# Kernel optimization log

Hardware: AMD Instinct MI355X
Metric: run time of the kernel (lower is better)

## Reference

```python
import jax, jax.numpy as jnp
import numpy as np

N, T, D_IN = 100000, 64, 2
H = 64            # hidden_channels
HEADS = 2
D_OUT = 2
E = 1000000
NEG_SLOPE = 0.2


def setup_inputs() -> dict:
    key = jax.random.key(0)
    ks = jax.random.split(key, 12)
    s = 0.05
    return {
        "x": jax.random.normal(ks[0], (N, T, D_IN), dtype=jnp.float32),
        "edge_index": jax.random.randint(ks[1], (2, E), 0, N, dtype=jnp.int64),
        # LSTM params (PyTorch gate order i,f,g,o)
        "w_ih": jax.random.normal(ks[2], (4 * H, D_IN), dtype=jnp.float32) * s,
        "w_hh": jax.random.normal(ks[3], (4 * H, H), dtype=jnp.float32) * s,
        "b_ih": jax.random.normal(ks[4], (4 * H,), dtype=jnp.float32) * s,
        "b_hh": jax.random.normal(ks[5], (4 * H,), dtype=jnp.float32) * s,
        # GATConv params (heads=2, concat=False)
        "gat_w": jax.random.normal(ks[6], (HEADS * H, H), dtype=jnp.float32) * s,
        "att_src": jax.random.normal(ks[7], (HEADS, H), dtype=jnp.float32) * s,
        "att_dst": jax.random.normal(ks[8], (HEADS, H), dtype=jnp.float32) * s,
        "gat_b": jax.random.normal(ks[9], (H,), dtype=jnp.float32) * s,
        # output head
        "lin_w": jax.random.normal(ks[10], (D_OUT, H), dtype=jnp.float32) * s,
        "lin_b": jax.random.normal(ks[11], (D_OUT,), dtype=jnp.float32) * s,
    }


def _lstm_last_h(x, w_ih, w_hh, b_ih, b_hh):
    """Single-layer batch_first LSTM; returns final hidden state [N, H]."""
    n = x.shape[0]
    # Precompute input projections for all timesteps: [T, N, 4H]
    x_proj = jnp.einsum('ntd,gd->tng', x, w_ih) + (b_ih + b_hh)

    def step(carry, xt):
        h, c = carry
        gates = xt + h @ w_hh.T                       # [N, 4H]
        i, f, g, o = jnp.split(gates, 4, axis=-1)
        i = jax.nn.sigmoid(i)
        f = jax.nn.sigmoid(f)
        g = jnp.tanh(g)
        o = jax.nn.sigmoid(o)
        c = f * c + i * g
        h = o * jnp.tanh(c)
        return (h, c), None

    h0 = jnp.zeros((n, H), dtype=x.dtype)
    (h_n, _), _ = jax.lax.scan(step, (h0, h0), x_proj)
    return h_n


def _gat_conv(x, edge_index, gat_w, att_src, att_dst, gat_b):
    """PyG GATConv, heads=2, concat=False (mean over heads), add_self_loops=True."""
    n = x.shape[0]
    # add self-loops
    loops = jnp.arange(n, dtype=edge_index.dtype)
    src = jnp.concatenate([edge_index[0], loops])
    dst = jnp.concatenate([edge_index[1], loops])

    xh = (x @ gat_w.T).reshape(n, HEADS, H)           # [N, heads, H]
    a_src = jnp.einsum('nhd,hd->nh', xh, att_src)     # [N, heads]
    a_dst = jnp.einsum('nhd,hd->nh', xh, att_dst)

    e = a_src[src] + a_dst[dst]                       # [Etot, heads]
    e = jax.nn.leaky_relu(e, NEG_SLOPE)
    # segment softmax over incoming edges of each destination node
    m = jax.ops.segment_max(e, dst, num_segments=n)
    e = jnp.exp(e - m[dst])
    z = jax.ops.segment_sum(e, dst, num_segments=n)
    alpha = e / z[dst]                                # [Etot, heads]

    msg = xh[src] * alpha[:, :, None]                 # [Etot, heads, H]
    out = jax.ops.segment_sum(msg, dst, num_segments=n)  # [N, heads, H]
    return out.mean(axis=1) + gat_b                   # concat=False -> mean


def reference(x, edge_index, w_ih, w_hh, b_ih, b_hh, gat_w, att_src, att_dst, gat_b, lin_w, lin_b):
    t_out = _lstm_last_h(x, w_ih, w_hh, b_ih, b_hh)           # [N, H]
    s_out = jax.nn.relu(_gat_conv(t_out, edge_index, gat_w, att_src, att_dst, gat_b))
    return jax.nn.sigmoid(s_out @ lin_w.T + lin_b)            # [N, D_OUT]
```

## Files before the change

kernel.cpp:

```cpp
#include <hip/hip_runtime.h>
#include <hip/hip_bf16.h>
#include <string.h>

#define NN 100000
#define TT 64
#define EE 1000000
#define LOG2E 1.44269504088896340736f

typedef __attribute__((ext_vector_type(8))) short bf16x8;
typedef __attribute__((ext_vector_type(4))) float f32x4;
typedef unsigned int u32;
typedef unsigned short u16;

__device__ __forceinline__ float bflo(u32 u) { return __builtin_bit_cast(float, u << 16); }
__device__ __forceinline__ float bfhi(u32 u) { return __builtin_bit_cast(float, u & 0xffff0000u); }
__device__ __forceinline__ u16 f2bf(float f) {
    u32 u = __builtin_bit_cast(u32, f);
    return (u16)((u + 0x7fffu + ((u >> 16) & 1u)) >> 16);
}
__device__ __forceinline__ u32 pack2(float a, float b) {
    return (u32)f2bf(a) | ((u32)f2bf(b) << 16);
}
__device__ __forceinline__ u32 pack2c(float a, float b) {
    __hip_bfloat162 t = __float22bfloat162_rn(make_float2(a, b));
    u32 r;
    __builtin_memcpy(&r, &t, 4);
    return r;
}
__device__ __forceinline__ float ex2(float x) { return __builtin_amdgcn_exp2f(x); }
__device__ __forceinline__ float fast_rcp(float x) { return __builtin_amdgcn_rcpf(x); }
#define MFMA16(A, B, C) __builtin_amdgcn_mfma_f32_16x16x32_bf16((A), (B), (C), 0, 0, 0)

__global__ __launch_bounds__(256)
__attribute__((amdgpu_waves_per_eu(2, 8))) void lstm_kernel(
    const float* __restrict__ x,
    const float* __restrict__ w_ih,
    const float* __restrict__ w_hh,
    const float* __restrict__ b_ih,
    const float* __restrict__ b_hh,
    u16* __restrict__ h_out)
{
    __shared__ __align__(16) u16 h_sh[2][64 * 72];
    __shared__ __align__(8) u32 x_lds[64 * 10];

    const int tid = threadIdx.x;
    const int wv = tid >> 6, lane = tid & 63;
    const int q = lane >> 4, cl = lane & 15;

    bf16x8 aI0, aI1, aF0, aF1, aG0, aG1, aO0, aO1;
    bf16x8 wxI, wxF, wxG, wxO;
    {
        const int rbase = wv * 16 + cl;
#define LOAD_A(D0, D1, G, SC)                                                \
        {                                                                    \
            const float* wr_ = w_hh + ((G) * 64 + rbase) * 64 + q * 8;       \
            float4 u0 = *(const float4*)(wr_);                               \
            float4 u1 = *(const float4*)(wr_ + 4);                           \
            uint4 t;                                                         \
            t.x = pack2(u0.x * (SC), u0.y * (SC));                           \
            t.y = pack2(u0.z * (SC), u0.w * (SC));                           \
            t.z = pack2(u1.x * (SC), u1.y * (SC));                           \
            t.w = pack2(u1.z * (SC), u1.w * (SC));                           \
            D0 = __builtin_bit_cast(bf16x8, t);                              \
            float4 v0 = *(const float4*)(wr_ + 32);                          \
            float4 v1 = *(const float4*)(wr_ + 36);                          \
            t.x = pack2(v0.x * (SC), v0.y * (SC));                           \
            t.y = pack2(v0.z * (SC), v0.w * (SC));                           \
            t.z = pack2(v1.x * (SC), v1.y * (SC));                           \
            t.w = pack2(v1.z * (SC), v1.w * (SC));                           \
            D1 = __builtin_bit_cast(bf16x8, t);                              \
        }
        LOAD_A(aI0, aI1, 0, LOG2E)
        LOAD_A(aF0, aF1, 1, LOG2E)
        LOAD_A(aG0, aG1, 2, 2.f * LOG2E)
        LOAD_A(aO0, aO1, 3, LOG2E)
#undef LOAD_A
#define LOAD_WT(D, G, SC)                                                    \
        {                                                                    \
            uint4 t = make_uint4(0u, 0u, 0u, 0u);                            \
            if (q == 0) {                                                    \
                int row = (G) * 64 + rbase;                                  \
                t.x = pack2(w_ih[row * 2 + 0] * (SC), w_ih[row * 2 + 1] * (SC)); \
                t.y = (u32)f2bf((b_ih[row] + b_hh[row]) * (SC));             \
            }                                                                \
            D = __builtin_bit_cast(bf16x8, t);                               \
        }
        LOAD_WT(wxI, 0, LOG2E)
        LOAD_WT(wxF, 1, LOG2E)
        LOAD_WT(wxG, 2, 2.f * LOG2E)
        LOAD_WT(wxO, 3, LOG2E)
#undef LOAD_WT
    }

    {
        u32* z = (u32*)h_sh[0];
        for (int i = tid; i < 2304; i += 256) z[i] = 0u;
    }

    const int nodeL = tid >> 2, f4 = tid & 3;
    int gnd = blockIdx.x * 64 + nodeL;
    gnd = gnd < NN ? gnd : NN - 1;
    const float* px = x + ((size_t)gnd * 64 + f4 * 2) * 2;
    float4 xr = *(const float4*)px;

    float cst[16];
#pragma unroll
    for (int i = 0; i < 16; ++i) cst[i] = 0.f;

    const f32x4 zero4 = {0.f, 0.f, 0.f, 0.f};
    const int rd16 = cl * 72 + q * 8;
    const int wr16 = cl * 72 + wv * 16 + q * 4;
    const int x16 = cl * 10;

    auto step = [&](const u16* hr_, u16* hw_, int SL) {
#pragma unroll
        for (int ct = 0; ct < 4; ++ct) {
            bf16x8 bh0 = *(const bf16x8*)(hr_ + ct * 1152 + rd16);
            bf16x8 bh1 = *(const bf16x8*)(hr_ + ct * 1152 + rd16 + 32);
            uint4 xt;
            xt.x = x_lds[ct * 160 + x16 + SL];
            xt.y = 0x00003F80u;
            xt.z = 0u; xt.w = 0u;
            bf16x8 bx = __builtin_bit_cast(bf16x8, xt);
            f32x4 accI, accF, accG, accO;
            accI = MFMA16(aI0, bh0, zero4);
            accI = MFMA16(aI1, bh1, accI);
            accI = MFMA16(wxI, bx, accI);
            accF = MFMA16(aF0, bh0, zero4);
            accF = MFMA16(aF1, bh1, accF);
            accF = MFMA16(wxF, bx, accF);
            accG = MFMA16(aG0, bh0, zero4);
            accG = MFMA16(aG1, bh1, accG);
            accG = MFMA16(wxG, bx, accG);
            accO = MFMA16(aO0, bh0, zero4);
            accO = MFMA16(aO1, bh1, accO);
            accO = MFMA16(wxO, bx, accO);
            float h0, h1, h2, h3;
#define ACT(R, HOUT)                                                       \
            {                                                              \
                float a_ = ex2(-accI[R]);                                  \
                float b_ = ex2(-accG[R]);                                  \
                float d_ = ex2(-accF[R]);                                  \
                float e_ = ex2(-accO[R]);                                  \
                float P = (1.f + a_) * (1.f + b_);                         \
                float D1 = 1.f + d_;                                       \
                float num = fmaf(cst[ct * 4 + R], P, (1.f - b_) * D1);     \
                float cc = num * fast_rcp(P * D1);                         \
                cst[ct * 4 + R] = cc;                                      \
                float t_ = ex2(-2.f * LOG2E * cc);                         \
                float R2 = (1.f + e_) * (1.f + t_);                        \
                HOUT = (1.f - t_) * fast_rcp(R2);                          \
            }
            ACT(0, h0) ACT(1, h1) ACT(2, h2) ACT(3, h3)
#undef ACT
            *((uint2*)(hw_ + ct * 1152 + wr16)) =
                make_uint2(pack2c(h0, h1), pack2c(h2, h3));
        }
    };

    for (int c = 0; c < 8; ++c) {
        *((uint2*)(x_lds + nodeL * 10 + f4 * 2)) =
            make_uint2(pack2c(xr.x, xr.y), pack2c(xr.z, xr.w));
        if (c < 7) xr = *(const float4*)(px + (c + 1) * 16);
        __syncthreads();
        for (int s2 = 0; s2 < 4; ++s2) {
            step(h_sh[0], h_sh[1], s2 * 2);
            __syncthreads();
            step(h_sh[1], h_sh[0], s2 * 2 + 1);
            __syncthreads();
        }
    }
#pragma unroll
    for (int i = 0; i < 8; ++i) {
        int id = i * 256 + tid;
        int row = id >> 5, col2 = (id & 31) * 2;
        int nd = blockIdx.x * 64 + row;
        if (nd < NN) {
            u32 u = *(const u32*)(h_sh[0] + row * 72 + col2);
            *((u32*)(h_out + (size_t)nd * 64 + col2)) = u;
        }
    }
}

__global__ void watt_kernel(const float* __restrict__ gat_w,
                            const float* __restrict__ att_src,
                            const float* __restrict__ att_dst,
                            float* __restrict__ watt) {
    int tid = threadIdx.x;
    int v = tid >> 6, k = tid & 63;
    int head = v & 1;
    const float* att = (v < 2) ? att_src : att_dst;
    float acc = 0.f;
#pragma unroll 8
    for (int d = 0; d < 64; ++d)
        acc = fmaf(att[head * 64 + d], gat_w[(head * 64 + d) * 64 + k], acc);
    watt[v * 64 + k] = acc;
}

__global__ __launch_bounds__(256, 2) void xh_kernel(
    const u16* __restrict__ h,
    const float* __restrict__ gat_w,
    const float* __restrict__ watt,
    u32* __restrict__ xh,
    float2* __restrict__ asrc,
    float2* __restrict__ adst)
{
    __shared__ __align__(16) u16 afrag[16 * 64 * 8];
    const int tid = threadIdx.x;
    const int wv = tid >> 6, lane = tid & 63;
    const int q = lane >> 4, cl = lane & 15;

    for (int f = wv; f < 16; f += 4) {
        int t = f >> 1, kh = f & 1;
        const float4* s4 = (const float4*)(gat_w + (t * 16 + cl) * 64 + kh * 32 + q * 8);
        float4 u0 = s4[0], u1 = s4[1];
        u16* d = afrag + (f * 64 + lane) * 8;
        d[0] = f2bf(u0.x); d[1] = f2bf(u0.y); d[2] = f2bf(u0.z); d[3] = f2bf(u0.w);
        d[4] = f2bf(u1.x); d[5] = f2bf(u1.y); d[6] = f2bf(u1.z); d[7] = f2bf(u1.w);
    }
    uint4 wa0u = make_uint4(0u, 0u, 0u, 0u), wa1u = wa0u;
    if (cl < 4) {
        const float* wp = watt + cl * 64;
        float4 a = *(const float4*)(wp + q * 8), b = *(const float4*)(wp + q * 8 + 4);
        wa0u = make_uint4(pack2(a.x, a.y), pack2(a.z, a.w), pack2(b.x, b.y), pack2(b.z, b.w));
        a = *(const float4*)(wp + 32 + q * 8); b = *(const float4*)(wp + 32 + q * 8 + 4);
        wa1u = make_uint4(pack2(a.x, a.y), pack2(a.z, a.w), pack2(b.x, b.y), pack2(b.z, b.w));
    }
    int node = blockIdx.x * 64 + wv * 16 + cl;
    node = node < NN ? node : NN - 1;
    const u16* hp = h + (size_t)node * 64;
    bf16x8 bh0 = *(const bf16x8*)(hp + q * 8);
    bf16x8 bh1 = *(const bf16x8*)(hp + 32 + q * 8);
    __syncthreads();

    const f32x4 zero4 = {0.f, 0.f, 0.f, 0.f};
    f32x4 acc[8];
#pragma unroll
    for (int t = 0; t < 8; ++t) {
        bf16x8 a0 = *(const bf16x8*)(afrag + ((t * 2 + 0) * 64 + lane) * 8);
        bf16x8 a1 = *(const bf16x8*)(afrag + ((t * 2 + 1) * 64 + lane) * 8);
        acc[t] = MFMA16(a0, bh0, zero4);
        acc[t] = MFMA16(a1, bh1, acc[t]);
    }
    f32x4 aw = MFMA16(__builtin_bit_cast(bf16x8, wa0u), bh0, zero4);
    aw = MFMA16(__builtin_bit_cast(bf16x8, wa1u), bh1, aw);

#pragma unroll
    for (int t = 0; t < 4; ++t) {
        uint4 o;
        o.x = pack2c(acc[t][0], acc[t + 4][0]);
        o.y = pack2c(acc[t][1], acc[t + 4][1]);
        o.z = pack2c(acc[t][2], acc[t + 4][2]);
        o.w = pack2c(acc[t][3], acc[t + 4][3]);
        *((uint4*)(xh + (size_t)node * 64 + t * 16 + q * 4)) = o;
    }
    if (q == 0) {
        asrc[node] = make_float2(aw[0], aw[1]);
        adst[node] = make_float2(aw[2], aw[3]);
    }
}

__global__ void hist_kernel(const int* __restrict__ ei, u32* __restrict__ deg) {
    int e = blockIdx.x * 256 + threadIdx.x;
    if (e < EE) atomicAdd(&deg[ei[EE + e]], 1u);
}

__global__ void scan1_kernel(u32* rp, u32* bsum) {
    __shared__ u32 tmp[256];
    int i = blockIdx.x * 256 + threadIdx.x;
    u32 v = (i < NN) ? rp[i] : 0u;
    tmp[threadIdx.x] = v;
    __syncthreads();
    for (int off = 1; off < 256; off <<= 1) {
        u32 t = (threadIdx.x >= (u32)off) ? tmp[threadIdx.x - off] : 0u;
        __syncthreads();
        tmp[threadIdx.x] += t;
        __syncthreads();
    }
    if (i < NN) rp[i] = tmp[threadIdx.x] - v;
    if (threadIdx.x == 255) bsum[blockIdx.x] = tmp[255];
}

__global__ void scan2_kernel(u32* bsum) {
    __shared__ u32 tmp[512];
    int tid = threadIdx.x;
    u32 v = (tid < 391) ? bsum[tid] : 0u;
    tmp[tid] = v;
    __syncthreads();
    for (int off = 1; off < 512; off <<= 1) {
        u32 t = (tid >= off) ? tmp[tid - off] : 0u;
        __syncthreads();
        tmp[tid] += t;
        __syncthreads();
    }
    if (tid < 391) bsum[tid] = tmp[tid] - v;
}

__global__ void scan3_kernel(u32* rp, const u32* __restrict__ bsum, u32* __restrict__ cursor) {
    int i = blockIdx.x * 256 + threadIdx.x;
    if (i < NN) {
        u32 v = rp[i] + bsum[blockIdx.x];
        rp[i] = v;
        cursor[i] = v;
    }
    if (blockIdx.x == 0 && threadIdx.x == 0) rp[NN] = EE;
}

__global__ void fill_kernel(const int* __restrict__ ei, u32* __restrict__ cursor,
                            int* __restrict__ csr) {
    int e = blockIdx.x * 256 + threadIdx.x;
    if (e < EE) {
        int s = ei[e], d = ei[EE + e];
        u32 p = atomicAdd(&cursor[d], 1u);
        csr[p] = s;
    }
}

__global__ __launch_bounds__(256) void gather_kernel(
    const u32* __restrict__ xh,
    const float2* __restrict__ asrc,
    const float2* __restrict__ adst,
    const u32* __restrict__ rp,
    const int* __restrict__ csr,
    const float* __restrict__ gat_b,
    const float* __restrict__ lin_w,
    const float* __restrict__ lin_b,
    float2* __restrict__ out)
{
    int wv = threadIdx.x >> 6, lane = threadIdx.x & 63;
    int node = blockIdx.x * 4 + wv;
    float2 ad = adst[node];
    float2 as = asrc[node];
    float e0 = as.x + ad.x; e0 = e0 > 0.f ? e0 : 0.2f * e0;
    float e1 = as.y + ad.y; e1 = e1 > 0.f ? e1 : 0.2f * e1;
    float w0 = ex2(LOG2E * e0);
    float w1 = ex2(LOG2E * e1);
    u32 u = xh[(size_t)node * 64 + lane];
    float acc0 = w0 * bflo(u), acc1 = w1 * bfhi(u);
    float z0 = w0, z1 = w1;
    u32 beg = rp[node], end = rp[node + 1];
    u32 p = beg;
    for (; p + 2 <= end; p += 2) {
        int s0 = csr[p], s1 = csr[p + 1];
        float2 A0 = asrc[s0], A1 = asrc[s1];
        u32 u0 = xh[(size_t)s0 * 64 + lane];
        u32 u1 = xh[(size_t)s1 * 64 + lane];
        float f00 = A0.x + ad.x; f00 = f00 > 0.f ? f00 : 0.2f * f00;
        float f01 = A0.y + ad.y; f01 = f01 > 0.f ? f01 : 0.2f * f01;
        float f10 = A1.x + ad.x; f10 = f10 > 0.f ? f10 : 0.2f * f10;
        float f11 = A1.y + ad.y; f11 = f11 > 0.f ? f11 : 0.2f * f11;
        float v00 = ex2(LOG2E * f00);
        float v01 = ex2(LOG2E * f01);
        float v10 = ex2(LOG2E * f10);
        float v11 = ex2(LOG2E * f11);
        acc0 = fmaf(v00, bflo(u0), acc0);
        acc1 = fmaf(v01, bfhi(u0), acc1);
        acc0 = fmaf(v10, bflo(u1), acc0);
        acc1 = fmaf(v11, bfhi(u1), acc1);
        z0 += v00 + v10;
        z1 += v01 + v11;
    }
    if (p < end) {
        int s = csr[p];
        float2 a2 = asrc[s];
        u32 uu = xh[(size_t)s * 64 + lane];
        float f0 = a2.x + ad.x; f0 = f0 > 0.f ? f0 : 0.2f * f0;
        float f1 = a2.y + ad.y; f1 = f1 > 0.f ? f1 : 0.2f * f1;
        float v0 = ex2(LOG2E * f0);
        float v1 = ex2(LOG2E * f1);
        acc0 = fmaf(v0, bflo(uu), acc0);
        acc1 = fmaf(v1, bfhi(uu), acc1);
        z0 += v0;
        z1 += v1;
    }
    float od = 0.5f * (acc0 * fast_rcp(z0) + acc1 * fast_rcp(z1)) + gat_b[lane];
    od = fmaxf(od, 0.f);
    float p0 = od * lin_w[lane];
    float p1 = od * lin_w[64 + lane];
#pragma unroll
    for (int off = 32; off > 0; off >>= 1) {
        p0 += __shfl_xor(p0, off);
        p1 += __shfl_xor(p1, off);
    }
    if (lane == 0) {
        float y0 = fast_rcp(1.f + ex2(-LOG2E * (p0 + lin_b[0])));
        float y1 = fast_rcp(1.f + ex2(-LOG2E * (p1 + lin_b[1])));
        out[node] = make_float2(y0, y1);
    }
}

extern "C" void kernel_launch(void* const* d_in, const int* in_sizes, int n_in,
                              void* d_out, int out_size, void* d_ws, size_t ws_size,
                              hipStream_t stream) {
    const float* x = (const float*)d_in[0];
    const int* ei = (const int*)d_in[1];
    const float* w_ih = (const float*)d_in[2];
    const float* w_hh = (const float*)d_in[3];
    const float* b_ih = (const float*)d_in[4];
    const float* b_hh = (const float*)d_in[5];
    const float* gat_w = (const float*)d_in[6];
    const float* att_src = (const float*)d_in[7];
    const float* att_dst = (const float*)d_in[8];
    const float* gat_b = (const float*)d_in[9];
    const float* lin_w = (const float*)d_in[10];
    const float* lin_b = (const float*)d_in[11];

    char* w = (char*)d_ws;
    u16* h = (u16*)(w);
    u32* xh = (u32*)(w + 12800000);
    float2* asrc = (float2*)(w + 38400000);
    float2* adst = (float2*)(w + 39200000);
    u32* rp = (u32*)(w + 40000000);
    u32* cursor = (u32*)(w + 40400128);
    u32* bsum = (u32*)(w + 40800128);
    int* csr = (int*)(w + 40802176);
    float* watt = (float*)(w + 44802176);

    (void)hipMemsetAsync(rp, 0, (NN + 1) * sizeof(u32), stream);
    lstm_kernel<<<1563, 256, 0, stream>>>(x, w_ih, w_hh, b_ih, b_hh, h);
    watt_kernel<<<1, 256, 0, stream>>>(gat_w, att_src, att_dst, watt);
    xh_kernel<<<1563, 256, 0, stream>>>(h, gat_w, watt, xh, asrc, adst);
    hist_kernel<<<(EE + 255) / 256, 256, 0, stream>>>(ei, rp);
    scan1_kernel<<<391, 256, 0, stream>>>(rp, bsum);
    scan2_kernel<<<1, 512, 0, stream>>>(bsum);
    scan3_kernel<<<391, 256, 0, stream>>>(rp, bsum, cursor);
    fill_kernel<<<(EE + 255) / 256, 256, 0, stream>>>(ei, cursor, csr);
    gather_kernel<<<NN / 4, 256, 0, stream>>>(xh, asrc, adst, rp, csr, gat_b, lin_w, lin_b,
                                              (float2*)d_out);
}
```

Measured before the change: 783.8 us.

## Process two independent 64-node groups per LSTM block to interleave recurrences

```diff
diff --git a/kernel.cpp b/kernel.cpp
--- a/kernel.cpp
+++ b/kernel.cpp
@@ -40,8 +40,8 @@
     const float* __restrict__ b_hh,
     u16* __restrict__ h_out)
 {
-    __shared__ __align__(16) u16 h_sh[2][64 * 72];
-    __shared__ __align__(8) u32 x_lds[64 * 10];
+    __shared__ __align__(16) u16 h_sh[2][2][64 * 72];
+    __shared__ __align__(8) u32 x_lds[2][64 * 10];
 
     const int tid = threadIdx.x;
     const int wv = tid >> 6, lane = tid & 63;
@@ -93,32 +93,37 @@
     }
 
     {
-        u32* z = (u32*)h_sh[0];
-        for (int i = tid; i < 2304; i += 256) z[i] = 0u;
+        u32* z0 = (u32*)h_sh[0][0];
+        u32* z1 = (u32*)h_sh[1][0];
+        for (int i = tid; i < 2304; i += 256) { z0[i] = 0u; z1[i] = 0u; }
     }
 
     const int nodeL = tid >> 2, f4 = tid & 3;
-    int gnd = blockIdx.x * 64 + nodeL;
-    gnd = gnd < NN ? gnd : NN - 1;
-    const float* px = x + ((size_t)gnd * 64 + f4 * 2) * 2;
-    float4 xr = *(const float4*)px;
-
-    float cst[16];
-#pragma unroll
-    for (int i = 0; i < 16; ++i) cst[i] = 0.f;
+    int gndA = blockIdx.x * 128 + nodeL;
+    int gndB = gndA + 64;
+    gndA = gndA < NN ? gndA : NN - 1;
+    gndB = gndB < NN ? gndB : NN - 1;
+    const float* pxA = x + ((size_t)gndA * 64 + f4 * 2) * 2;
+    const float* pxB = x + ((size_t)gndB * 64 + f4 * 2) * 2;
+    float4 xrA = *(const float4*)pxA;
+    float4 xrB = *(const float4*)pxB;
+
+    float cstA[16], cstB[16];
+#pragma unroll
+    for (int i = 0; i < 16; ++i) { cstA[i] = 0.f; cstB[i] = 0.f; }
 
     const f32x4 zero4 = {0.f, 0.f, 0.f, 0.f};
     const int rd16 = cl * 72 + q * 8;
     const int wr16 = cl * 72 + wv * 16 + q * 4;
     const int x16 = cl * 10;
 
-    auto step = [&](const u16* hr_, u16* hw_, int SL) {
+    auto step = [&](const u16* hr_, u16* hw_, int SL, float* cst_, const u32* xl_) {
 #pragma unroll
         for (int ct = 0; ct < 4; ++ct) {
             bf16x8 bh0 = *(const bf16x8*)(hr_ + ct * 1152 + rd16);
             bf16x8 bh1 = *(const bf16x8*)(hr_ + ct * 1152 + rd16 + 32);
             uint4 xt;
-            xt.x = x_lds[ct * 160 + x16 + SL];
+            xt.x = xl_[ct * 160 + x16 + SL];
             xt.y = 0x00003F80u;
             xt.z = 0u; xt.w = 0u;
             bf16x8 bx = __builtin_bit_cast(bf16x8, xt);
@@ -144,9 +149,9 @@
                 float e_ = ex2(-accO[R]);                                  \
                 float P = (1.f + a_) * (1.f + b_);                         \
                 float D1 = 1.f + d_;                                       \
-                float num = fmaf(cst[ct * 4 + R], P, (1.f - b_) * D1);     \
+                float num = fmaf(cst_[ct * 4 + R], P, (1.f - b_) * D1);    \
                 float cc = num * fast_rcp(P * D1);                         \
-                cst[ct * 4 + R] = cc;                                      \
+                cst_[ct * 4 + R] = cc;                                     \
                 float t_ = ex2(-2.f * LOG2E * cc);                         \
                 float R2 = (1.f + e_) * (1.f + t_);                        \
                 HOUT = (1.f - t_) * fast_rcp(R2);                          \
@@ -159,25 +164,35 @@
     };
 
     for (int c = 0; c < 8; ++c) {
-        *((uint2*)(x_lds + nodeL * 10 + f4 * 2)) =
-            make_uint2(pack2c(xr.x, xr.y), pack2c(xr.z, xr.w));
-        if (c < 7) xr = *(const float4*)(px + (c + 1) * 16);
+        *((uint2*)(x_lds[0] + nodeL * 10 + f4 * 2)) =
+            make_uint2(pack2c(xrA.x, xrA.y), pack2c(xrA.z, xrA.w));
+        *((uint2*)(x_lds[1] + nodeL * 10 + f4 * 2)) =
+            make_uint2(pack2c(xrB.x, xrB.y), pack2c(xrB.z, xrB.w));
+        if (c < 7) {
+            xrA = *(const float4*)(pxA + (c + 1) * 16);
+            xrB = *(const float4*)(pxB + (c + 1) * 16);
+        }
         __syncthreads();
         for (int s2 = 0; s2 < 4; ++s2) {
-            step(h_sh[0], h_sh[1], s2 * 2);
+            step(h_sh[0][0], h_sh[0][1], s2 * 2, cstA, x_lds[0]);
+            step(h_sh[1][0], h_sh[1][1], s2 * 2, cstB, x_lds[1]);
             __syncthreads();
-            step(h_sh[1], h_sh[0], s2 * 2 + 1);
+            step(h_sh[0][1], h_sh[0][0], s2 * 2 + 1, cstA, x_lds[0]);
+            step(h_sh[1][1], h_sh[1][0], s2 * 2 + 1, cstB, x_lds[1]);
             __syncthreads();
         }
     }
 #pragma unroll
-    for (int i = 0; i < 8; ++i) {
-        int id = i * 256 + tid;
-        int row = id >> 5, col2 = (id & 31) * 2;
-        int nd = blockIdx.x * 64 + row;
-        if (nd < NN) {
-            u32 u = *(const u32*)(h_sh[0] + row * 72 + col2);
-            *((u32*)(h_out + (size_t)nd * 64 + col2)) = u;
+    for (int g = 0; g < 2; ++g) {
+#pragma unroll
+        for (int i = 0; i < 8; ++i) {
+            int id = i * 256 + tid;
+            int row = id >> 5, col2 = (id & 31) * 2;
+            int nd = blockIdx.x * 128 + g * 64 + row;
+            if (nd < NN) {
+                u32 u = *(const u32*)(h_sh[g][0] + row * 72 + col2);
+                *((u32*)(h_out + (size_t)nd * 64 + col2)) = u;
+            }
         }
     }
 }
@@ -417,7 +432,7 @@
     float* watt = (float*)(w + 44802176);
 
     (void)hipMemsetAsync(rp, 0, (NN + 1) * sizeof(u32), stream);
-    lstm_kernel<<<1563, 256, 0, stream>>>(x, w_ih, w_hh, b_ih, b_hh, h);
+    lstm_kernel<<<782, 256, 0, stream>>>(x, w_ih, w_hh, b_ih, b_hh, h);
     watt_kernel<<<1, 256, 0, stream>>>(gat_w, att_src, att_dst, watt);
     xh_kernel<<<1563, 256, 0, stream>>>(h, gat_w, watt, xh, asrc, adst);
     hist_kernel<<<(EE + 255) / 256, 256, 0, stream>>>(ei, rp);
```

After: 876.2 us. +11.8%, slower.

## Merge edge-histogram and CSR-fill work into LSTM and xh kernels as extra blocks

Applied to the files above, without the earlier changes.

```diff
diff --git a/kernel.cpp b/kernel.cpp
--- a/kernel.cpp
+++ b/kernel.cpp
@@ -6,6 +6,10 @@
 #define TT 64
 #define EE 1000000
 #define LOG2E 1.44269504088896340736f
+
+#define LSTM_NB 1563
+#define EDGE_NB 977
+#define XH_NB 1563
 
 typedef __attribute__((ext_vector_type(8))) short bf16x8;
 typedef __attribute__((ext_vector_type(4))) float f32x4;
@@ -31,19 +35,53 @@
 __device__ __forceinline__ float fast_rcp(float x) { return __builtin_amdgcn_rcpf(x); }
 #define MFMA16(A, B, C) __builtin_amdgcn_mfma_f32_16x16x32_bf16((A), (B), (C), 0, 0, 0)
 
+__device__ __forceinline__ void bar_lds() {
+    asm volatile("s_waitcnt lgkmcnt(0)" ::: "memory");
+    __builtin_amdgcn_s_barrier();
+}
+
 __global__ __launch_bounds__(256)
-__attribute__((amdgpu_waves_per_eu(2, 8))) void lstm_kernel(
+__attribute__((amdgpu_waves_per_eu(2, 8))) void lstm_hist_kernel(
     const float* __restrict__ x,
     const float* __restrict__ w_ih,
     const float* __restrict__ w_hh,
     const float* __restrict__ b_ih,
     const float* __restrict__ b_hh,
-    u16* __restrict__ h_out)
+    u16* __restrict__ h_out,
+    const int* __restrict__ ei,
+    u32* __restrict__ deg,
+    const float* __restrict__ gat_w,
+    const float* __restrict__ att_src,
+    const float* __restrict__ att_dst,
+    float* __restrict__ watt)
 {
     __shared__ __align__(16) u16 h_sh[2][64 * 72];
     __shared__ __align__(8) u32 x_lds[64 * 10];
 
     const int tid = threadIdx.x;
+
+    if (blockIdx.x >= LSTM_NB) {
+        const int bb = blockIdx.x - LSTM_NB;
+        if (bb == EDGE_NB) {
+            int v = tid >> 6, k = tid & 63;
+            int head = v & 1;
+            const float* att = (v < 2) ? att_src : att_dst;
+            float acc = 0.f;
+#pragma unroll 8
+            for (int d = 0; d < 64; ++d)
+                acc = fmaf(att[head * 64 + d], gat_w[(head * 64 + d) * 64 + k], acc);
+            watt[v * 64 + k] = acc;
+            return;
+        }
+        const int base = bb * 1024 + tid;
+#pragma unroll
+        for (int i = 0; i < 4; ++i) {
+            int e = base + i * 256;
+            if (e < EE) atomicAdd(&deg[ei[EE + e]], 1u);
+        }
+        return;
+    }
+
     const int wv = tid >> 6, lane = tid & 63;
     const int q = lane >> 4, cl = lane & 15;
 
@@ -162,12 +200,12 @@
         *((uint2*)(x_lds + nodeL * 10 + f4 * 2)) =
             make_uint2(pack2c(xr.x, xr.y), pack2c(xr.z, xr.w));
         if (c < 7) xr = *(const float4*)(px + (c + 1) * 16);
-        __syncthreads();
+        bar_lds();
         for (int s2 = 0; s2 < 4; ++s2) {
             step(h_sh[0], h_sh[1], s2 * 2);
-            __syncthreads();
+            bar_lds();
             step(h_sh[1], h_sh[0], s2 * 2 + 1);
-            __syncthreads();
+            bar_lds();
         }
     }
 #pragma unroll
@@ -182,31 +220,35 @@
     }
 }
 
-__global__ void watt_kernel(const float* __restrict__ gat_w,
-                            const float* __restrict__ att_src,
-                            const float* __restrict__ att_dst,
-                            float* __restrict__ watt) {
-    int tid = threadIdx.x;
-    int v = tid >> 6, k = tid & 63;
-    int head = v & 1;
-    const float* att = (v < 2) ? att_src : att_dst;
-    float acc = 0.f;
-#pragma unroll 8
-    for (int d = 0; d < 64; ++d)
-        acc = fmaf(att[head * 64 + d], gat_w[(head * 64 + d) * 64 + k], acc);
-    watt[v * 64 + k] = acc;
-}
-
-__global__ __launch_bounds__(256, 2) void xh_kernel(
+__global__ __launch_bounds__(256, 2) void xh_fill_kernel(
     const u16* __restrict__ h,
     const float* __restrict__ gat_w,
     const float* __restrict__ watt,
     u32* __restrict__ xh,
     float2* __restrict__ asrc,
-    float2* __restrict__ adst)
+    float2* __restrict__ adst,
+    const int* __restrict__ ei,
+    u32* __restrict__ cursor,
+    int* __restrict__ csr)
 {
     __shared__ __align__(16) u16 afrag[16 * 64 * 8];
     const int tid = threadIdx.x;
+
+    if (blockIdx.x >= XH_NB) {
+        const int bb = blockIdx.x - XH_NB;
+        const int base = bb * 1024 + tid;
+#pragma unroll
+        for (int i = 0; i < 4; ++i) {
+            int e = base + i * 256;
+            if (e < EE) {
+                int s = ei[e], d = ei[EE + e];
+                u32 p = atomicAdd(&cursor[d], 1u);
+                csr[p] = s;
+            }
+        }
+        return;
+    }
+
     const int wv = tid >> 6, lane = tid & 63;
     const int q = lane >> 4, cl = lane & 15;
 
@@ -258,11 +300,6 @@
         asrc[node] = make_float2(aw[0], aw[1]);
         adst[node] = make_float2(aw[2], aw[3]);
     }
-}
-
-__global__ void hist_kernel(const int* __restrict__ ei, u32* __restrict__ deg) {
-    int e = blockIdx.x * 256 + threadIdx.x;
-    if (e < EE) atomicAdd(&deg[ei[EE + e]], 1u);
 }
 
 __global__ void scan1_kernel(u32* rp, u32* bsum) {
@@ -304,16 +341,6 @@
         cursor[i] = v;
     }
     if (blockIdx.x == 0 && threadIdx.x == 0) rp[NN] = EE;
-}
-
-__global__ void fill_kernel(const int* __restrict__ ei, u32* __restrict__ cursor,
-                            int* __restrict__ csr) {
-    int e = blockIdx.x * 256 + threadIdx.x;
-    if (e < EE) {
-        int s = ei[e], d = ei[EE + e];
-        u32 p = atomicAdd(&cursor[d], 1u);
-        csr[p] = s;
-    }
 }
 
 __global__ __launch_bounds__(256) void gather_kernel(
@@ -417,14 +444,13 @@
     float* watt = (float*)(w + 44802176);
 
     (void)hipMemsetAsync(rp, 0, (NN + 1) * sizeof(u32), stream);
-    lstm_kernel<<<1563, 256, 0, stream>>>(x, w_ih, w_hh, b_ih, b_hh, h);
-    watt_kernel<<<1, 256, 0, stream>>>(gat_w, att_src, att_dst, watt);
-    xh_kernel<<<1563, 256, 0, stream>>>(h, gat_w, watt, xh, asrc, adst);
-    hist_kernel<<<(EE + 255) / 256, 256, 0, stream>>>(ei, rp);
+    lstm_hist_kernel<<<LSTM_NB + EDGE_NB + 1, 256, 0, stream>>>(
+        x, w_ih, w_hh, b_ih, b_hh, h, ei, rp, gat_w, att_src, att_dst, watt);
     scan1_kernel<<<391, 256, 0, stream>>>(rp, bsum);
     scan2_kernel<<<1, 512, 0, stream>>>(bsum);
     scan3_kernel<<<391, 256, 0, stream>>>(rp, bsum, cursor);
-    fill_kernel<<<(EE + 255) / 256, 256, 0, stream>>>(ei, cursor, csr);
+    xh_fill_kernel<<<XH_NB + EDGE_NB, 256, 0, stream>>>(
+        h, gat_w, watt, xh, asrc, adst, ei, cursor, csr);
     gather_kernel<<<NN / 4, 256, 0, stream>>>(xh, asrc, adst, rp, csr, gat_b, lin_w, lin_b,
                                               (float2*)d_out);
 }
```

After: 739.6 us. 5.6% less time.
